# Performance work log

Hardware: AMD Instinct MI355X
Metric: run time of the kernel (lower is better)

Reference implementation:

```python
import jax, jax.numpy as jnp
import numpy as np

B, S, H, I = 2, 1024, 1024, 4096
G, E = 4, 4
NE = G * E
CAP = 1024


def setup_inputs() -> dict:
    key = jax.random.key(0)
    ks = jax.random.split(key, 6)
    return {
        "hidden_states": jax.random.normal(ks[0], (B, S, H), jnp.float32),
        "group_router_w": jax.random.normal(ks[1], (G, H), jnp.float32) * 0.02,
        "expert_router_w": jax.random.normal(ks[2], (G, E, H), jnp.float32) * 0.02,
        "gate_w": jax.random.normal(ks[3], (NE, I, H), jnp.float32) * 0.02,
        "up_w": jax.random.normal(ks[4], (NE, I, H), jnp.float32) * 0.02,
        "down_w": jax.random.normal(ks[5], (NE, H, I), jnp.float32) * 0.02,
    }


def _forward(x, gw, erw, Wg, Wu, Wd):
    b, s, h = x.shape
    T = b * s
    xf = x.reshape(T, h)
    # level 1: group routing (fp32 softmax, top-2 groups)
    group_logits = xf @ gw.T                                        # [T,G]
    group_probs = jax.nn.softmax(group_logits.astype(jnp.float32), axis=-1)
    top_gp, top_gi = jax.lax.top_k(group_probs, 2)                  # [T,2]
    # level 2: per-group expert routing (top-1 expert within group)
    expert_logits = jnp.einsum('th,geh->tge', xf, erw)              # [T,G,E]
    expert_probs = jax.nn.softmax(expert_logits.astype(jnp.float32), axis=-1)
    e_idx = jnp.argmax(expert_probs, axis=-1)                       # [T,G]
    e_prob = jnp.max(expert_probs, axis=-1)                         # [T,G]
    sel_e = jnp.take_along_axis(e_idx, top_gi, axis=1)              # [T,2]
    sel_p = jnp.take_along_axis(e_prob, top_gi, axis=1)             # [T,2]
    eid = (top_gi * E + sel_e).reshape(-1)                          # [2T] global expert id
    wgt = (top_gp * sel_p).reshape(-1)                              # [2T] combine weight
    x2 = jnp.repeat(xf, 2, axis=0)                                  # [2T,H], slot-major per token
    # capacity-based dispatch: position within expert via cumsum of one-hot
    onehot = jax.nn.one_hot(eid, NE, dtype=jnp.int32)               # [2T,NE]
    pos = (jnp.cumsum(onehot, axis=0) * onehot).sum(axis=1) - 1     # [2T]
    keep = pos < CAP
    pos_c = jnp.where(keep, pos, CAP)                               # overflow -> dummy slot
    buf = jnp.zeros((NE, CAP + 1, h), x.dtype).at[eid, pos_c].set(x2)
    # grouped-GEMM gated FFN (SwiGLU) over all experts at once
    gate = jax.nn.silu(jnp.einsum('ech,eih->eci', buf, Wg))
    up = jnp.einsum('ech,eih->eci', buf, Wu)
    yexp = jnp.einsum('eci,ehi->ech', gate * up, Wd)                # [NE,CAP+1,H]
    # combine: gather back and weight; dropped tokens get zero weight
    y = yexp[eid, pos_c] * jnp.where(keep, wgt, 0.0)[:, None].astype(x.dtype)
    out = (y[0::2] + y[1::2]).reshape(b, s, h)
    aux_loss = jnp.zeros((), jnp.float32)  # aux-loss accumulation truncated in source; initialized to 0
    return out, aux_loss


def reference(hidden_states, group_router_w, expert_router_w, gate_w, up_w, down_w):
    return _forward(hidden_states, group_router_w, expert_router_w, gate_w, up_w, down_w)
```

## Files before the change

kernel.cpp:

```cpp
#include <hip/hip_runtime.h>
#include <hip/hip_bf16.h>

typedef float f32x4 __attribute__((ext_vector_type(4)));
typedef __bf16 bf16x8 __attribute__((ext_vector_type(8)));

#define H 1024
#define II 4096
#define NE 16
#define CAP 1024
#define NTOK 2048
#define NSLOT 4096

__global__ __launch_bounds__(256) void k_route(
    const float* __restrict__ x, const float* __restrict__ gw,
    const float* __restrict__ erw, int* __restrict__ eid,
    float* __restrict__ wgt) {
  int t = blockIdx.x * 4 + (threadIdx.x >> 6);
  int lane = threadIdx.x & 63;
  const float* xr = x + (size_t)t * H;
  double acc[20];
#pragma unroll
  for (int j = 0; j < 20; j++) acc[j] = 0.0;
  for (int it = 0; it < 16; ++it) {
    int h = it * 64 + lane;
    float xv = xr[h];
#pragma unroll
    for (int g = 0; g < 4; ++g) acc[g] += (double)xv * (double)gw[g * H + h];
#pragma unroll
    for (int j = 0; j < 16; ++j)
      acc[4 + j] += (double)xv * (double)erw[j * H + h];
  }
#pragma unroll
  for (int j = 0; j < 20; ++j) {
    double v = acc[j];
#pragma unroll
    for (int o = 32; o > 0; o >>= 1) v += __shfl_down(v, o, 64);
    acc[j] = v;
  }
  if (lane == 0) {
    float gl[4];
#pragma unroll
    for (int g = 0; g < 4; g++) gl[g] = (float)acc[g];
    int g1 = 0;
#pragma unroll
    for (int g = 1; g < 4; g++)
      if (gl[g] > gl[g1]) g1 = g;
    int g2 = (g1 == 0) ? 1 : 0;
#pragma unroll
    for (int g = 0; g < 4; g++)
      if (g != g1 && gl[g] > gl[g2]) g2 = g;
    float gm = fmaxf(fmaxf(gl[0], gl[1]), fmaxf(gl[2], gl[3]));
    float s = 0.f;
#pragma unroll
    for (int g = 0; g < 4; g++) s += expf(gl[g] - gm);
    float p[2] = {expf(gl[g1] - gm) / s, expf(gl[g2] - gm) / s};
    int gs[2] = {g1, g2};
#pragma unroll
    for (int k = 0; k < 2; k++) {
      int g = gs[k];
      float el[4];
#pragma unroll
      for (int e2 = 0; e2 < 4; e2++) el[e2] = (float)acc[4 + g * 4 + e2];
      int eb = 0;
#pragma unroll
      for (int e2 = 1; e2 < 4; e2++)
        if (el[e2] > el[eb]) eb = e2;
      float es = 0.f;
#pragma unroll
      for (int e2 = 0; e2 < 4; e2++) es += expf(el[e2] - el[eb]);
      eid[2 * t + k] = g * 4 + eb;
      wgt[2 * t + k] = p[k] * (1.f / es);
    }
  }
}

__global__ __launch_bounds__(1024) void k_scan(const int* __restrict__ eid,
                                               int* __restrict__ perm,
                                               int* __restrict__ cnt,
                                               int* __restrict__ kept) {
  int wid = threadIdx.x >> 6;
  int lane = threadIdx.x & 63;
  int base = 0;
  for (int it = 0; it < 64; ++it) {
    int slot = it * 64 + lane;
    int e = eid[slot];
    unsigned long long m = __ballot(e == wid);
    if (e == wid) {
      int pos = base + __popcll(m & ((1ull << lane) - 1ull));
      if (pos < CAP) {
        perm[wid * CAP + pos] = slot;
        kept[slot] = 1;
      } else {
        kept[slot] = 0;
      }
    }
    base += __popcll(m);
  }
  if (lane == 0) cnt[wid] = (base < CAP) ? base : CAP;
}

__global__ __launch_bounds__(256) void k_cvtx(const float* __restrict__ x,
                                              __bf16* __restrict__ xb) {
  size_t i = ((size_t)blockIdx.x * 256 + threadIdx.x) * 8;
  f32x4 a = *(const f32x4*)(x + i);
  f32x4 b = *(const f32x4*)(x + i + 4);
  bf16x8 o;
#pragma unroll
  for (int j = 0; j < 4; j++) {
    o[j] = (__bf16)a[j];
    o[j + 4] = (__bf16)b[j];
  }
  *(bf16x8*)(xb + i) = o;
}

#define FENCE_BAR()                                    \
  asm volatile("s_waitcnt lgkmcnt(0)" ::: "memory");   \
  __builtin_amdgcn_sched_barrier(0);                   \
  __builtin_amdgcn_s_barrier();

__global__ __launch_bounds__(512, 2) void k_gateup(
    const __bf16* __restrict__ xb, const float* __restrict__ Wg,
    const float* __restrict__ Wu, const int* __restrict__ perm,
    const int* __restrict__ cnt, __bf16* __restrict__ act) {
  __shared__ __bf16 As[128 * 32];
  __shared__ __bf16 Gs[128 * 32];
  __shared__ __bf16 Us[128 * 32];
  __shared__ int slotArr[128];
  const int e = blockIdx.z, nt = blockIdx.x, rt = blockIdx.y;
  const int ce = cnt[e];
  if (rt * 128 >= ce) return;
  const int tid = threadIdx.x, lane = tid & 63, wid = tid >> 6;
  if (tid < 128) {
    int ridx = rt * 128 + tid;
    slotArr[tid] = perm[e * CAP + (ridx < ce ? ridx : 0)];
  }
  __syncthreads();
  const int srow = tid >> 2;
  const int sch = tid & 3;
  const int wrOff = srow * 32 + (sch ^ ((srow >> 1) & 3)) * 8;
  const __bf16* pA = xb + (size_t)(slotArr[srow] >> 1) * H + sch * 8;
  const size_t ew = (size_t)e * II * H + (size_t)(nt * 128 + srow) * H;
  const float* pG = Wg + ew + sch * 8;
  const float* pU = Wu + ew + sch * 8;
  const int wm = wid >> 1, wn = wid & 1;
  f32x4 accG[2][4], accU[2][4];
#pragma unroll
  for (int m = 0; m < 2; m++)
#pragma unroll
    for (int n = 0; n < 4; n++)
#pragma unroll
      for (int i = 0; i < 4; i++) {
        accG[m][n][i] = 0.f;
        accU[m][n][i] = 0.f;
      }
  bf16x8 sA0, sA1;
  f32x4 sG00, sG01, sU00, sU01, sG10, sG11, sU10, sU11;

#define GU_LOADS(A8, G0, G1, U0, U1, T)     \
  {                                         \
    const int ko = (T) * 32;                \
    A8 = *(const bf16x8*)(pA + ko);         \
    G0 = *(const f32x4*)(pG + ko);          \
    G1 = *(const f32x4*)(pG + ko + 4);      \
    U0 = *(const f32x4*)(pU + ko);          \
    U1 = *(const f32x4*)(pU + ko + 4);      \
  }
#define GU_WRITE(A8, G0, G1, U0, U1)        \
  {                                         \
    *(bf16x8*)&As[wrOff] = A8;              \
    bf16x8 fg, fu;                          \
    _Pragma("unroll") for (int i = 0; i < 4; i++) { \
      fg[i] = (__bf16)G0[i];                \
      fg[i + 4] = (__bf16)G1[i];            \
      fu[i] = (__bf16)U0[i];                \
      fu[i + 4] = (__bf16)U1[i];            \
    }                                       \
    *(bf16x8*)&Gs[wrOff] = fg;              \
    *(bf16x8*)&Us[wrOff] = fu;              \
  }
#define GU_COMPUTE()                                                     \
  {                                                                      \
    bf16x8 aF[2], gF[4], uF[4];                                          \
    _Pragma("unroll") for (int m = 0; m < 2; m++) {                      \
      int r = wm * 32 + m * 16 + (lane & 15);                            \
      int c = (lane >> 4) ^ ((r >> 1) & 3);                              \
      aF[m] = *(const bf16x8*)&As[r * 32 + c * 8];                       \
    }                                                                    \
    _Pragma("unroll") for (int n = 0; n < 4; n++) {                      \
      int r = wn * 64 + n * 16 + (lane & 15);                            \
      int c = (lane >> 4) ^ ((r >> 1) & 3);                              \
      gF[n] = *(const bf16x8*)&Gs[r * 32 + c * 8];                       \
      uF[n] = *(const bf16x8*)&Us[r * 32 + c * 8];                       \
    }                                                                    \
    _Pragma("unroll") for (int m = 0; m < 2; m++)                        \
        _Pragma("unroll") for (int n = 0; n < 4; n++) {                  \
      accG[m][n] = __builtin_amdgcn_mfma_f32_16x16x32_bf16(              \
          aF[m], gF[n], accG[m][n], 0, 0, 0);                            \
      accU[m][n] = __builtin_amdgcn_mfma_f32_16x16x32_bf16(              \
          aF[m], uF[n], accU[m][n], 0, 0, 0);                            \
    }                                                                    \
  }

  GU_LOADS(sA0, sG00, sG01, sU00, sU01, 0);
  GU_LOADS(sA1, sG10, sG11, sU10, sU11, 1);
  GU_WRITE(sA0, sG00, sG01, sU00, sU01);
  FENCE_BAR();
  for (int tt = 0; tt < 16; ++tt) {
    const int t0 = 2 * tt;
    if (t0 + 2 < 32) GU_LOADS(sA0, sG00, sG01, sU00, sU01, t0 + 2);
    GU_COMPUTE();
    FENCE_BAR();
    GU_WRITE(sA1, sG10, sG11, sU10, sU11);
    FENCE_BAR();
    if (t0 + 3 < 32) GU_LOADS(sA1, sG10, sG11, sU10, sU11, t0 + 3);
    GU_COMPUTE();
    if (t0 + 2 < 32) {
      FENCE_BAR();
      GU_WRITE(sA0, sG00, sG01, sU00, sU01);
      FENCE_BAR();
    }
  }
  const int colB = nt * 128 + wn * 64;
#pragma unroll
  for (int m = 0; m < 2; m++)
#pragma unroll
    for (int n = 0; n < 4; n++)
#pragma unroll
      for (int i = 0; i < 4; i++) {
        int row = wm * 32 + m * 16 + (lane >> 4) * 4 + i;
        if (rt * 128 + row < ce) {
          int slot = slotArr[row];
          float g = accG[m][n][i];
          float u = accU[m][n][i];
          float a = (g / (1.f + __expf(-g))) * u;
          act[(size_t)slot * II + colB + n * 16 + (lane & 15)] = (__bf16)a;
        }
      }
}

__global__ __launch_bounds__(512, 2) void k_down(
    const __bf16* __restrict__ act, const float* __restrict__ Wd,
    const int* __restrict__ perm, const int* __restrict__ cnt,
    const float* __restrict__ wgt, float* __restrict__ y) {
  __shared__ __bf16 As[128 * 64];
  __shared__ __bf16 Ws[128 * 64];
  __shared__ int slotArr[128];
  const int e = blockIdx.z, nt = blockIdx.x, rt = blockIdx.y;
  const int ce = cnt[e];
  if (rt * 128 >= ce) return;
  const int tid = threadIdx.x, lane = tid & 63, wid = tid >> 6;
  if (tid < 128) {
    int ridx = rt * 128 + tid;
    slotArr[tid] = perm[e * CAP + (ridx < ce ? ridx : 0)];
  }
  __syncthreads();
  const int srow = tid >> 2;
  const int c0 = tid & 3;
  const int wr0 = srow * 64 + (c0 ^ (srow & 7)) * 8;
  const int wr1 = srow * 64 + ((c0 + 4) ^ (srow & 7)) * 8;
  const __bf16* pA = act + (size_t)slotArr[srow] * II + c0 * 8;
  const float* pW =
      Wd + (size_t)e * H * II + (size_t)(nt * 128 + srow) * II + c0 * 8;
  const int wm = wid >> 1, wn = wid & 1;
  f32x4 acc[2][4];
#pragma unroll
  for (int m = 0; m < 2; m++)
#pragma unroll
    for (int n = 0; n < 4; n++)
#pragma unroll
      for (int i = 0; i < 4; i++) acc[m][n][i] = 0.f;
  bf16x8 dA00, dA01, dA10, dA11;
  f32x4 dW000, dW001, dW010, dW011, dW100, dW101, dW110, dW111;

#define DN_LOADS(A0, A1, W00, W01, W10, W11, T) \
  {                                             \
    const int ko = (T) * 64;                    \
    A0 = *(const bf16x8*)(pA + ko);             \
    A1 = *(const bf16x8*)(pA + ko + 32);        \
    W00 = *(const f32x4*)(pW + ko);             \
    W01 = *(const f32x4*)(pW + ko + 4);         \
    W10 = *(const f32x4*)(pW + ko + 32);        \
    W11 = *(const f32x4*)(pW + ko + 36);        \
  }
#define DN_WRITE(A0, A1, W00, W01, W10, W11)    \
  {                                             \
    *(bf16x8*)&As[wr0] = A0;                    \
    *(bf16x8*)&As[wr1] = A1;                    \
    bf16x8 f0, f1;                              \
    _Pragma("unroll") for (int i = 0; i < 4; i++) { \
      f0[i] = (__bf16)W00[i];                   \
      f0[i + 4] = (__bf16)W01[i];               \
      f1[i] = (__bf16)W10[i];                   \
      f1[i + 4] = (__bf16)W11[i];               \
    }                                           \
    *(bf16x8*)&Ws[wr0] = f0;                    \
    *(bf16x8*)&Ws[wr1] = f1;                    \
  }
#define DN_COMPUTE()                                                     \
  {                                                                      \
    _Pragma("unroll") for (int kk = 0; kk < 2; ++kk) {                   \
      bf16x8 aF[2], wF[4];                                               \
      _Pragma("unroll") for (int m = 0; m < 2; m++) {                    \
        int r = wm * 32 + m * 16 + (lane & 15);                          \
        int c = (kk * 4 + (lane >> 4)) ^ (r & 7);                        \
        aF[m] = *(const bf16x8*)&As[r * 64 + c * 8];                     \
      }                                                                  \
      _Pragma("unroll") for (int n = 0; n < 4; n++) {                    \
        int r = wn * 64 + n * 16 + (lane & 15);                          \
        int c = (kk * 4 + (lane >> 4)) ^ (r & 7);                        \
        wF[n] = *(const bf16x8*)&Ws[r * 64 + c * 8];                     \
      }                                                                  \
      _Pragma("unroll") for (int m = 0; m < 2; m++)                      \
          _Pragma("unroll") for (int n = 0; n < 4; n++)                  \
              acc[m][n] = __builtin_amdgcn_mfma_f32_16x16x32_bf16(       \
                  aF[m], wF[n], acc[m][n], 0, 0, 0);                     \
    }                                                                    \
  }

  DN_LOADS(dA00, dA01, dW000, dW001, dW010, dW011, 0);
  DN_LOADS(dA10, dA11, dW100, dW101, dW110, dW111, 1);
  DN_WRITE(dA00, dA01, dW000, dW001, dW010, dW011);
  FENCE_BAR();
  for (int tt = 0; tt < 32; ++tt) {
    const int t0 = 2 * tt;
    if (t0 + 2 < 64) DN_LOADS(dA00, dA01, dW000, dW001, dW010, dW011, t0 + 2);
    DN_COMPUTE();
    FENCE_BAR();
    DN_WRITE(dA10, dA11, dW100, dW101, dW110, dW111);
    FENCE_BAR();
    if (t0 + 3 < 64) DN_LOADS(dA10, dA11, dW100, dW101, dW110, dW111, t0 + 3);
    DN_COMPUTE();
    if (t0 + 2 < 64) {
      FENCE_BAR();
      DN_WRITE(dA00, dA01, dW000, dW001, dW010, dW011);
      FENCE_BAR();
    }
  }
  const int colB = nt * 128 + wn * 64;
#pragma unroll
  for (int m = 0; m < 2; m++)
#pragma unroll
    for (int n = 0; n < 4; n++)
#pragma unroll
      for (int i = 0; i < 4; i++) {
        int row = wm * 32 + m * 16 + (lane >> 4) * 4 + i;
        if (rt * 128 + row < ce) {
          int slot = slotArr[row];
          y[(size_t)slot * H + colB + n * 16 + (lane & 15)] =
              wgt[slot] * acc[m][n][i];
        }
      }
}

__global__ __launch_bounds__(256) void k_combine(const float* __restrict__ y,
                                                 const int* __restrict__ kept,
                                                 float* __restrict__ out) {
  int t = blockIdx.x, tid = threadIdx.x;
  const f32x4* y0 = (const f32x4*)(y + (size_t)(2 * t) * H);
  const f32x4* y1 = (const f32x4*)(y + (size_t)(2 * t + 1) * H);
  f32x4 a, b;
#pragma unroll
  for (int i = 0; i < 4; i++) {
    a[i] = 0.f;
    b[i] = 0.f;
  }
  if (kept[2 * t]) a = y0[tid];
  if (kept[2 * t + 1]) b = y1[tid];
  ((f32x4*)out)[(size_t)t * 256 + tid] = a + b;
  if (t == 0 && tid == 0) out[(size_t)NTOK * H] = 0.f;
}

extern "C" void kernel_launch(void* const* d_in, const int* in_sizes, int n_in,
                              void* d_out, int out_size, void* d_ws,
                              size_t ws_size, hipStream_t stream) {
  const float* x = (const float*)d_in[0];
  const float* gw = (const float*)d_in[1];
  const float* erw = (const float*)d_in[2];
  const float* Wg = (const float*)d_in[3];
  const float* Wu = (const float*)d_in[4];
  const float* Wd = (const float*)d_in[5];
  float* out = (float*)d_out;
  char* ws = (char*)d_ws;
  int* eid = (int*)(ws);
  float* wgt = (float*)(ws + (16 << 10));
  int* kept = (int*)(ws + (32 << 10));
  int* cnt = (int*)(ws + (48 << 10));
  int* perm = (int*)(ws + (64 << 10));
  __bf16* act = (__bf16*)(ws + (128 << 10));
  float* yb = (float*)(ws + (128 << 10) + (size_t)NSLOT * II * 2);
  __bf16* xb = (__bf16*)(ws + (128 << 10) + (size_t)NSLOT * II * 2 +
                         (size_t)NSLOT * H * 4);

  k_route<<<NTOK / 4, 256, 0, stream>>>(x, gw, erw, eid, wgt);
  k_scan<<<1, 1024, 0, stream>>>(eid, perm, cnt, kept);
  k_cvtx<<<NTOK * H / 8 / 256, 256, 0, stream>>>(x, xb);
  k_gateup<<<dim3(32, 8, 16), 512, 0, stream>>>(xb, Wg, Wu, perm, cnt, act);
  k_down<<<dim3(8, 8, 16), 512, 0, stream>>>(act, Wd, perm, cnt, wgt, yb);
  k_combine<<<NTOK, 256, 0, stream>>>(yb, kept, out);
}
```

Before: 371.8 us.

## Load fp32 weights straight into MFMA B-fragments, staging only activations in LDS

Both grouped GEMM kernels stop staging the fp32 weights through shared memory. Each wave now loads its own 32 weight rows from global memory directly in MFMA fragment layout, converts them to bf16 in registers, and shares only the token tile (A) through a double-buffered, padded LDS array. Blocks shrink to 256 threads, and each wave covers all 128 rows by 32 columns. The aim is to cut LDS traffic and barrier overhead on the weight stream, at the cost of more accumulator registers, lower occupancy in gate/up (launch bounds 1), and less coalesced weight loads.

```diff
diff --git a/kernel.cpp b/kernel.cpp
--- a/kernel.cpp
+++ b/kernel.cpp
@@ -118,236 +118,250 @@
   __builtin_amdgcn_sched_barrier(0);                   \
   __builtin_amdgcn_s_barrier();
 
-__global__ __launch_bounds__(512, 2) void k_gateup(
+#define MFMA_BF16(A, B, C) __builtin_amdgcn_mfma_f32_16x16x32_bf16(A, B, C, 0, 0, 0)
+
+#define ASTRIDE 40
+
+__global__ __launch_bounds__(256, 1) void k_gateup(
     const __bf16* __restrict__ xb, const float* __restrict__ Wg,
     const float* __restrict__ Wu, const int* __restrict__ perm,
     const int* __restrict__ cnt, __bf16* __restrict__ act) {
-  __shared__ __bf16 As[128 * 32];
-  __shared__ __bf16 Gs[128 * 32];
-  __shared__ __bf16 Us[128 * 32];
+  __shared__ __bf16 As[2][128 * ASTRIDE];
   __shared__ int slotArr[128];
   const int e = blockIdx.z, nt = blockIdx.x, rt = blockIdx.y;
   const int ce = cnt[e];
-  if (rt * 128 >= ce) return;
-  const int tid = threadIdx.x, lane = tid & 63, wid = tid >> 6;
+  if (ce <= 0 || rt * 128 >= ce) return;
+  const int tid = threadIdx.x, lane = tid & 63, w = tid >> 6;
   if (tid < 128) {
     int ridx = rt * 128 + tid;
     slotArr[tid] = perm[e * CAP + (ridx < ce ? ridx : 0)];
   }
   __syncthreads();
-  const int srow = tid >> 2;
-  const int sch = tid & 3;
-  const int wrOff = srow * 32 + (sch ^ ((srow >> 1) & 3)) * 8;
-  const __bf16* pA = xb + (size_t)(slotArr[srow] >> 1) * H + sch * 8;
-  const size_t ew = (size_t)e * II * H + (size_t)(nt * 128 + srow) * H;
-  const float* pG = Wg + ew + sch * 8;
-  const float* pU = Wu + ew + sch * 8;
-  const int wm = wid >> 1, wn = wid & 1;
-  f32x4 accG[2][4], accU[2][4];
-#pragma unroll
-  for (int m = 0; m < 2; m++)
-#pragma unroll
-    for (int n = 0; n < 4; n++)
+  const int arow = tid >> 1, ahk = tid & 1;
+  const __bf16* pA = xb + (size_t)(slotArr[arow] >> 1) * H + ahk * 16;
+  const int wAoff = arow * ASTRIDE + ahk * 16;
+  const int l15 = lane & 15, lk = lane >> 4;
+  const size_t ewg = (size_t)e * II * H;
+  const int rb = nt * 128 + w * 32 + l15;
+  const float* pG0 = Wg + ewg + (size_t)rb * H + lk * 8;
+  const float* pG1 = pG0 + (size_t)16 * H;
+  const float* pU0 = Wu + ewg + (size_t)rb * H + lk * 8;
+  const float* pU1 = pU0 + (size_t)16 * H;
+
+  f32x4 accG[8][2], accU[8][2];
+#pragma unroll
+  for (int m = 0; m < 8; m++)
+#pragma unroll
+    for (int n = 0; n < 2; n++)
 #pragma unroll
       for (int i = 0; i < 4; i++) {
         accG[m][n][i] = 0.f;
         accU[m][n][i] = 0.f;
       }
-  bf16x8 sA0, sA1;
-  f32x4 sG00, sG01, sU00, sU01, sG10, sG11, sU10, sU11;
-
-#define GU_LOADS(A8, G0, G1, U0, U1, T)     \
-  {                                         \
-    const int ko = (T) * 32;                \
-    A8 = *(const bf16x8*)(pA + ko);         \
-    G0 = *(const f32x4*)(pG + ko);          \
-    G1 = *(const f32x4*)(pG + ko + 4);      \
-    U0 = *(const f32x4*)(pU + ko);          \
-    U1 = *(const f32x4*)(pU + ko + 4);      \
-  }
-#define GU_WRITE(A8, G0, G1, U0, U1)        \
-  {                                         \
-    *(bf16x8*)&As[wrOff] = A8;              \
-    bf16x8 fg, fu;                          \
-    _Pragma("unroll") for (int i = 0; i < 4; i++) { \
-      fg[i] = (__bf16)G0[i];                \
-      fg[i + 4] = (__bf16)G1[i];            \
-      fu[i] = (__bf16)U0[i];                \
-      fu[i + 4] = (__bf16)U1[i];            \
-    }                                       \
-    *(bf16x8*)&Gs[wrOff] = fg;              \
-    *(bf16x8*)&Us[wrOff] = fu;              \
-  }
-#define GU_COMPUTE()                                                     \
-  {                                                                      \
-    bf16x8 aF[2], gF[4], uF[4];                                          \
-    _Pragma("unroll") for (int m = 0; m < 2; m++) {                      \
-      int r = wm * 32 + m * 16 + (lane & 15);                            \
-      int c = (lane >> 4) ^ ((r >> 1) & 3);                              \
-      aF[m] = *(const bf16x8*)&As[r * 32 + c * 8];                       \
-    }                                                                    \
-    _Pragma("unroll") for (int n = 0; n < 4; n++) {                      \
-      int r = wn * 64 + n * 16 + (lane & 15);                            \
-      int c = (lane >> 4) ^ ((r >> 1) & 3);                              \
-      gF[n] = *(const bf16x8*)&Gs[r * 32 + c * 8];                       \
-      uF[n] = *(const bf16x8*)&Us[r * 32 + c * 8];                       \
-    }                                                                    \
-    _Pragma("unroll") for (int m = 0; m < 2; m++)                        \
-        _Pragma("unroll") for (int n = 0; n < 4; n++) {                  \
-      accG[m][n] = __builtin_amdgcn_mfma_f32_16x16x32_bf16(              \
-          aF[m], gF[n], accG[m][n], 0, 0, 0);                            \
-      accU[m][n] = __builtin_amdgcn_mfma_f32_16x16x32_bf16(              \
-          aF[m], uF[n], accU[m][n], 0, 0, 0);                            \
-    }                                                                    \
-  }
-
-  GU_LOADS(sA0, sG00, sG01, sU00, sU01, 0);
-  GU_LOADS(sA1, sG10, sG11, sU10, sU11, 1);
-  GU_WRITE(sA0, sG00, sG01, sU00, sU01);
+
+#define DECLB(P) f32x4 P##0l, P##0h, P##1l, P##1h, P##2l, P##2h, P##3l, P##3h
+#define LOADB(P, T)                          \
+  {                                          \
+    const int ko = (T) * 32;                 \
+    P##0l = *(const f32x4*)(pG0 + ko);       \
+    P##0h = *(const f32x4*)(pG0 + ko + 4);   \
+    P##1l = *(const f32x4*)(pG1 + ko);       \
+    P##1h = *(const f32x4*)(pG1 + ko + 4);   \
+    P##2l = *(const f32x4*)(pU0 + ko);       \
+    P##2h = *(const f32x4*)(pU0 + ko + 4);   \
+    P##3l = *(const f32x4*)(pU1 + ko);       \
+    P##3h = *(const f32x4*)(pU1 + ko + 4);   \
+  }
+#define CVTB(P, bg0, bg1, bu0, bu1)                  \
+  {                                                  \
+    _Pragma("unroll") for (int i = 0; i < 4; i++) {  \
+      bg0[i] = (__bf16)P##0l[i];                     \
+      bg0[i + 4] = (__bf16)P##0h[i];                 \
+      bg1[i] = (__bf16)P##1l[i];                     \
+      bg1[i + 4] = (__bf16)P##1h[i];                 \
+      bu0[i] = (__bf16)P##2l[i];                     \
+      bu0[i + 4] = (__bf16)P##2h[i];                 \
+      bu1[i] = (__bf16)P##3l[i];                     \
+      bu1[i + 4] = (__bf16)P##3h[i];                 \
+    }                                                \
+  }
+#define LOADA(S0, S1, T)                             \
+  {                                                  \
+    S0 = *(const bf16x8*)(pA + (T) * 32);            \
+    S1 = *(const bf16x8*)(pA + (T) * 32 + 8);        \
+  }
+#define WRITEA(BUF, S0, S1)                          \
+  {                                                  \
+    *(bf16x8*)&As[BUF][wAoff] = S0;                  \
+    *(bf16x8*)&As[BUF][wAoff + 8] = S1;              \
+  }
+#define GU_MFMA(CB, bg0, bg1, bu0, bu1)                           \
+  {                                                               \
+    _Pragma("unroll") for (int m = 0; m < 8; m++) {               \
+      bf16x8 aF =                                                 \
+          *(const bf16x8*)&As[CB][(m * 16 + l15) * ASTRIDE + lk * 8]; \
+      accG[m][0] = MFMA_BF16(aF, bg0, accG[m][0]);                \
+      accG[m][1] = MFMA_BF16(aF, bg1, accG[m][1]);                \
+      accU[m][0] = MFMA_BF16(aF, bu0, accU[m][0]);                \
+      accU[m][1] = MFMA_BF16(aF, bu1, accU[m][1]);                \
+    }                                                             \
+  }
+
+  DECLB(Ba);
+  DECLB(Bb);
+  bf16x8 aSa0, aSa1, aSb0, aSb1;
+
+  LOADA(aSa0, aSa1, 0);
+  LOADB(Ba, 0);
+  LOADA(aSb0, aSb1, 1);
+  LOADB(Bb, 1);
+  WRITEA(0, aSa0, aSa1);
+  LOADA(aSa0, aSa1, 2);
   FENCE_BAR();
+
   for (int tt = 0; tt < 16; ++tt) {
-    const int t0 = 2 * tt;
-    if (t0 + 2 < 32) GU_LOADS(sA0, sG00, sG01, sU00, sU01, t0 + 2);
-    GU_COMPUTE();
-    FENCE_BAR();
-    GU_WRITE(sA1, sG10, sG11, sU10, sU11);
-    FENCE_BAR();
-    if (t0 + 3 < 32) GU_LOADS(sA1, sG10, sG11, sU10, sU11, t0 + 3);
-    GU_COMPUTE();
-    if (t0 + 2 < 32) {
+    const int t0 = 2 * tt, t1 = t0 + 1;
+    {
+      if (t0 + 1 < 32) WRITEA(1, aSb0, aSb1);
+      if (t0 + 3 < 32) LOADA(aSb0, aSb1, t0 + 3);
+      bf16x8 bg0, bg1, bu0, bu1;
+      CVTB(Ba, bg0, bg1, bu0, bu1);
+      if (t0 + 2 < 32) LOADB(Ba, t0 + 2);
+      GU_MFMA(0, bg0, bg1, bu0, bu1);
       FENCE_BAR();
-      GU_WRITE(sA0, sG00, sG01, sU00, sU01);
-      FENCE_BAR();
-    }
-  }
-  const int colB = nt * 128 + wn * 64;
-#pragma unroll
-  for (int m = 0; m < 2; m++)
-#pragma unroll
-    for (int n = 0; n < 4; n++)
+    }
+    {
+      if (t1 + 1 < 32) WRITEA(0, aSa0, aSa1);
+      if (t1 + 3 < 32) LOADA(aSa0, aSa1, t1 + 3);
+      bf16x8 bg0, bg1, bu0, bu1;
+      CVTB(Bb, bg0, bg1, bu0, bu1);
+      if (t1 + 2 < 32) LOADB(Bb, t1 + 2);
+      GU_MFMA(1, bg0, bg1, bu0, bu1);
+      if (t1 < 31) FENCE_BAR();
+    }
+  }
+  const int colB = nt * 128 + w * 32;
+#pragma unroll
+  for (int m = 0; m < 8; m++)
+#pragma unroll
+    for (int j = 0; j < 2; j++)
 #pragma unroll
       for (int i = 0; i < 4; i++) {
-        int row = wm * 32 + m * 16 + (lane >> 4) * 4 + i;
+        int row = m * 16 + lk * 4 + i;
         if (rt * 128 + row < ce) {
           int slot = slotArr[row];
-          float g = accG[m][n][i];
-          float u = accU[m][n][i];
+          float g = accG[m][j][i];
+          float u = accU[m][j][i];
           float a = (g / (1.f + __expf(-g))) * u;
-          act[(size_t)slot * II + colB + n * 16 + (lane & 15)] = (__bf16)a;
+          act[(size_t)slot * II + colB + j * 16 + l15] = (__bf16)a;
         }
       }
 }
 
-__global__ __launch_bounds__(512, 2) void k_down(
+__global__ __launch_bounds__(256, 2) void k_down(
     const __bf16* __restrict__ act, const float* __restrict__ Wd,
     const int* __restrict__ perm, const int* __restrict__ cnt,
     const float* __restrict__ wgt, float* __restrict__ y) {
-  __shared__ __bf16 As[128 * 64];
-  __shared__ __bf16 Ws[128 * 64];
+  __shared__ __bf16 As[2][128 * ASTRIDE];
   __shared__ int slotArr[128];
   const int e = blockIdx.z, nt = blockIdx.x, rt = blockIdx.y;
   const int ce = cnt[e];
-  if (rt * 128 >= ce) return;
-  const int tid = threadIdx.x, lane = tid & 63, wid = tid >> 6;
+  if (ce <= 0 || rt * 128 >= ce) return;
+  const int tid = threadIdx.x, lane = tid & 63, w = tid >> 6;
   if (tid < 128) {
     int ridx = rt * 128 + tid;
     slotArr[tid] = perm[e * CAP + (ridx < ce ? ridx : 0)];
   }
   __syncthreads();
-  const int srow = tid >> 2;
-  const int c0 = tid & 3;
-  const int wr0 = srow * 64 + (c0 ^ (srow & 7)) * 8;
-  const int wr1 = srow * 64 + ((c0 + 4) ^ (srow & 7)) * 8;
-  const __bf16* pA = act + (size_t)slotArr[srow] * II + c0 * 8;
-  const float* pW =
-      Wd + (size_t)e * H * II + (size_t)(nt * 128 + srow) * II + c0 * 8;
-  const int wm = wid >> 1, wn = wid & 1;
-  f32x4 acc[2][4];
-#pragma unroll
-  for (int m = 0; m < 2; m++)
-#pragma unroll
-    for (int n = 0; n < 4; n++)
+  const int arow = tid >> 1, ahk = tid & 1;
+  const __bf16* pA = act + (size_t)slotArr[arow] * II + ahk * 16;
+  const int wAoff = arow * ASTRIDE + ahk * 16;
+  const int l15 = lane & 15, lk = lane >> 4;
+  const int rb = nt * 128 + w * 32 + l15;
+  const float* pB0 = Wd + (size_t)e * H * II + (size_t)rb * II + lk * 8;
+  const float* pB1 = pB0 + (size_t)16 * II;
+
+  f32x4 acc[8][2];
+#pragma unroll
+  for (int m = 0; m < 8; m++)
+#pragma unroll
+    for (int n = 0; n < 2; n++)
 #pragma unroll
       for (int i = 0; i < 4; i++) acc[m][n][i] = 0.f;
-  bf16x8 dA00, dA01, dA10, dA11;
-  f32x4 dW000, dW001, dW010, dW011, dW100, dW101, dW110, dW111;
-
-#define DN_LOADS(A0, A1, W00, W01, W10, W11, T) \
-  {                                             \
-    const int ko = (T) * 64;                    \
-    A0 = *(const bf16x8*)(pA + ko);             \
-    A1 = *(const bf16x8*)(pA + ko + 32);        \
-    W00 = *(const f32x4*)(pW + ko);             \
-    W01 = *(const f32x4*)(pW + ko + 4);         \
-    W10 = *(const f32x4*)(pW + ko + 32);        \
-    W11 = *(const f32x4*)(pW + ko + 36);        \
-  }
-#define DN_WRITE(A0, A1, W00, W01, W10, W11)    \
-  {                                             \
-    *(bf16x8*)&As[wr0] = A0;                    \
-    *(bf16x8*)&As[wr1] = A1;                    \
-    bf16x8 f0, f1;                              \
-    _Pragma("unroll") for (int i = 0; i < 4; i++) { \
-      f0[i] = (__bf16)W00[i];                   \
-      f0[i + 4] = (__bf16)W01[i];               \
-      f1[i] = (__bf16)W10[i];                   \
-      f1[i + 4] = (__bf16)W11[i];               \
-    }                                           \
-    *(bf16x8*)&Ws[wr0] = f0;                    \
-    *(bf16x8*)&Ws[wr1] = f1;                    \
-  }
-#define DN_COMPUTE()                                                     \
-  {                                                                      \
-    _Pragma("unroll") for (int kk = 0; kk < 2; ++kk) {                   \
-      bf16x8 aF[2], wF[4];                                               \
-      _Pragma("unroll") for (int m = 0; m < 2; m++) {                    \
-        int r = wm * 32 + m * 16 + (lane & 15);                          \
-        int c = (kk * 4 + (lane >> 4)) ^ (r & 7);                        \
-        aF[m] = *(const bf16x8*)&As[r * 64 + c * 8];                     \
-      }                                                                  \
-      _Pragma("unroll") for (int n = 0; n < 4; n++) {                    \
-        int r = wn * 64 + n * 16 + (lane & 15);                          \
-        int c = (kk * 4 + (lane >> 4)) ^ (r & 7);                        \
-        wF[n] = *(const bf16x8*)&Ws[r * 64 + c * 8];                     \
-      }                                                                  \
-      _Pragma("unroll") for (int m = 0; m < 2; m++)                      \
-          _Pragma("unroll") for (int n = 0; n < 4; n++)                  \
-              acc[m][n] = __builtin_amdgcn_mfma_f32_16x16x32_bf16(       \
-                  aF[m], wF[n], acc[m][n], 0, 0, 0);                     \
-    }                                                                    \
-  }
-
-  DN_LOADS(dA00, dA01, dW000, dW001, dW010, dW011, 0);
-  DN_LOADS(dA10, dA11, dW100, dW101, dW110, dW111, 1);
-  DN_WRITE(dA00, dA01, dW000, dW001, dW010, dW011);
+
+#define DECLBD(P) f32x4 P##0l, P##0h, P##1l, P##1h
+#define LOADBD(P, T)                         \
+  {                                          \
+    const int ko = (T) * 32;                 \
+    P##0l = *(const f32x4*)(pB0 + ko);       \
+    P##0h = *(const f32x4*)(pB0 + ko + 4);   \
+    P##1l = *(const f32x4*)(pB1 + ko);       \
+    P##1h = *(const f32x4*)(pB1 + ko + 4);   \
+  }
+#define CVTBD(P, b0, b1)                             \
+  {                                                  \
+    _Pragma("unroll") for (int i = 0; i < 4; i++) {  \
+      b0[i] = (__bf16)P##0l[i];                      \
+      b0[i + 4] = (__bf16)P##0h[i];                  \
+      b1[i] = (__bf16)P##1l[i];                      \
+      b1[i + 4] = (__bf16)P##1h[i];                  \
+    }                                                \
+  }
+#define DN_MFMA(CB, b0, b1)                                       \
+  {                                                               \
+    _Pragma("unroll") for (int m = 0; m < 8; m++) {               \
+      bf16x8 aF =                                                 \
+          *(const bf16x8*)&As[CB][(m * 16 + l15) * ASTRIDE + lk * 8]; \
+      acc[m][0] = MFMA_BF16(aF, b0, acc[m][0]);                   \
+      acc[m][1] = MFMA_BF16(aF, b1, acc[m][1]);                   \
+    }                                                             \
+  }
+
+  DECLBD(Ba);
+  DECLBD(Bb);
+  bf16x8 aSa0, aSa1, aSb0, aSb1;
+
+  LOADA(aSa0, aSa1, 0);
+  LOADBD(Ba, 0);
+  LOADA(aSb0, aSb1, 1);
+  LOADBD(Bb, 1);
+  WRITEA(0, aSa0, aSa1);
+  LOADA(aSa0, aSa1, 2);
   FENCE_BAR();
-  for (int tt = 0; tt < 32; ++tt) {
-    const int t0 = 2 * tt;
-    if (t0 + 2 < 64) DN_LOADS(dA00, dA01, dW000, dW001, dW010, dW011, t0 + 2);
-    DN_COMPUTE();
-    FENCE_BAR();
-    DN_WRITE(dA10, dA11, dW100, dW101, dW110, dW111);
-    FENCE_BAR();
-    if (t0 + 3 < 64) DN_LOADS(dA10, dA11, dW100, dW101, dW110, dW111, t0 + 3);
-    DN_COMPUTE();
-    if (t0 + 2 < 64) {
+
+  for (int tt = 0; tt < 64; ++tt) {
+    const int t0 = 2 * tt, t1 = t0 + 1;
+    {
+      if (t0 + 1 < 128) WRITEA(1, aSb0, aSb1);
+      if (t0 + 3 < 128) LOADA(aSb0, aSb1, t0 + 3);
+      bf16x8 b0, b1;
+      CVTBD(Ba, b0, b1);
+      if (t0 + 2 < 128) LOADBD(Ba, t0 + 2);
+      DN_MFMA(0, b0, b1);
       FENCE_BAR();
-      DN_WRITE(dA00, dA01, dW000, dW001, dW010, dW011);
-      FENCE_BAR();
-    }
-  }
-  const int colB = nt * 128 + wn * 64;
-#pragma unroll
-  for (int m = 0; m < 2; m++)
-#pragma unroll
-    for (int n = 0; n < 4; n++)
+    }
+    {
+      if (t1 + 1 < 128) WRITEA(0, aSa0, aSa1);
+      if (t1 + 3 < 128) LOADA(aSa0, aSa1, t1 + 3);
+      bf16x8 b0, b1;
+      CVTBD(Bb, b0, b1);
+      if (t1 + 2 < 128) LOADBD(Bb, t1 + 2);
+      DN_MFMA(1, b0, b1);
+      if (t1 < 127) FENCE_BAR();
+    }
+  }
+  const int colB = nt * 128 + w * 32;
+#pragma unroll
+  for (int m = 0; m < 8; m++)
+#pragma unroll
+    for (int j = 0; j < 2; j++)
 #pragma unroll
       for (int i = 0; i < 4; i++) {
-        int row = wm * 32 + m * 16 + (lane >> 4) * 4 + i;
+        int row = m * 16 + lk * 4 + i;
         if (rt * 128 + row < ce) {
           int slot = slotArr[row];
-          y[(size_t)slot * H + colB + n * 16 + (lane & 15)] =
-              wgt[slot] * acc[m][n][i];
+          y[(size_t)slot * H + colB + j * 16 + l15] =
+              wgt[slot] * acc[m][j][i];
         }
       }
 }
@@ -394,7 +408,7 @@
   k_route<<<NTOK / 4, 256, 0, stream>>>(x, gw, erw, eid, wgt);
   k_scan<<<1, 1024, 0, stream>>>(eid, perm, cnt, kept);
   k_cvtx<<<NTOK * H / 8 / 256, 256, 0, stream>>>(x, xb);
-  k_gateup<<<dim3(32, 8, 16), 512, 0, stream>>>(xb, Wg, Wu, perm, cnt, act);
-  k_down<<<dim3(8, 8, 16), 512, 0, stream>>>(act, Wd, perm, cnt, wgt, yb);
+  k_gateup<<<dim3(32, 8, 16), 256, 0, stream>>>(xb, Wg, Wu, perm, cnt, act);
+  k_down<<<dim3(8, 8, 16), 256, 0, stream>>>(act, Wd, perm, cnt, wgt, yb);
   k_combine<<<NTOK, 256, 0, stream>>>(yb, kept, out);
 }
```

Result: slower. 572.6 us (+54.0%).
